# Kernel optimization log

Hardware: AMD Instinct MI355X
Metric: run time of the kernel (lower is better)

## Reference

```python
import jax, jax.numpy as jnp
import numpy as np

C = 128          # num_channels
HID = 256        # mlp hidden = 2*C
HEAD_DIM = 16    # C // num_heads (8)
SCALE = 1.0 / np.sqrt(HEAD_DIM)
EPS = 1e-5


def _linear_init(key, fan_in, fan_out):
    kw, kb = jax.random.split(key)
    s = 1.0 / np.sqrt(fan_in)
    w = jax.random.uniform(kw, (fan_in, fan_out), minval=-s, maxval=s, dtype=jnp.float32)
    b = jax.random.uniform(kb, (fan_out,), minval=-s, maxval=s, dtype=jnp.float32)
    return w, b


def setup_inputs() -> dict:
    key = jax.random.key(0)
    ks = jax.random.split(key, 8)
    x = jax.random.normal(ks[0], (4, C, 64, 64), dtype=jnp.float32)
    wq, bq = _linear_init(ks[1], C, C)
    wk, bk = _linear_init(ks[2], C, C)
    wv, bv = _linear_init(ks[3], C, C)
    wo, bo = _linear_init(ks[4], C, C)
    w1, b1 = _linear_init(ks[5], C, HID)
    w2, b2 = _linear_init(ks[6], HID, C)
    return {
        "x": x,
        "ln1_w": jnp.ones((C,), jnp.float32), "ln1_b": jnp.zeros((C,), jnp.float32),
        "wq": wq, "bq": bq, "wk": wk, "bk": bk, "wv": wv, "bv": bv,
        "wo": wo, "bo": bo,
        "ln2_w": jnp.ones((C,), jnp.float32), "ln2_b": jnp.zeros((C,), jnp.float32),
        "w1": w1, "b1": b1, "w2": w2, "b2": b2,
    }


def _layernorm(x, w, b):
    mu = jnp.mean(x, axis=-1, keepdims=True)
    var = jnp.mean(jnp.square(x - mu), axis=-1, keepdims=True)
    return (x - mu) * jax.lax.rsqrt(var + EPS) * w + b


def reference(x, ln1_w, ln1_b, wq, bq, wk, bk, wv, bv, wo, bo, ln2_w, ln2_b, w1, b1, w2, b2):
    B, Cc, H, W = x.shape
    t = x.reshape(B, Cc, H * W).transpose(0, 2, 1)  # [B, S, C]
    xl = _layernorm(t, ln1_w, ln1_b)
    q = xl @ wq + bq
    k = xl @ wk + bk
    v = xl @ wv + bv
    scores = jnp.einsum('bqc,bkc->bqk', q, k) * SCALE  # [B, S, S]
    # Faithful to source: softmax over dim=1 (the QUERY axis).
    attn = jax.nn.softmax(scores, axis=1)
    att_out = jnp.einsum('bqk,bkc->bqc', attn, v) @ wo + bo
    t = att_out + t
    m = _layernorm(t, ln2_w, ln2_b) @ w1 + b1
    m = jax.nn.gelu(m, approximate=False) @ w2 + b2
    t = jax.nn.gelu(m, approximate=False) + t  # second GELU per source
    return t.transpose(0, 2, 1).reshape(B, Cc, H, W)
```

## Files before the change

kernel.cpp:

```cpp
#include <hip/hip_runtime.h>
#include <math.h>

#define S 4096
#define CNUM 128
#define BATCH 4
#define MTOT (BATCH * S)
#define SCLOG2E 0.36067376022224085f
#define EPSLN 1e-5f
#define KSPLIT 8
#define QSPLIT 8

typedef __attribute__((ext_vector_type(8))) short bf16x8;
typedef __attribute__((ext_vector_type(4))) float f32x4;
typedef __attribute__((ext_vector_type(4))) unsigned int u32x4;

__device__ __forceinline__ float gelu_exact(float x) {
    return 0.5f * x * (1.0f + erff(x * 0.7071067811865476f));
}

__device__ __forceinline__ unsigned short f2b(float f) {
    union { float f; unsigned int u; } v; v.f = f;
    unsigned int r = (v.u + 0x7FFFu + ((v.u >> 16) & 1u)) >> 16;
    return (unsigned short)r;
}
__device__ __forceinline__ unsigned short f2b_ru(float f) {
    return (unsigned short)((__float_as_uint(f) + 0x8000u) >> 16);
}
__device__ __forceinline__ float b2f(unsigned short u) {
    return __uint_as_float((unsigned)u << 16);
}

__device__ __forceinline__ void gl_lds16(const void* g, void* l) {
    __builtin_amdgcn_global_load_lds(
        (__attribute__((address_space(1))) void*)g,
        (__attribute__((address_space(3))) void*)l, 16, 0, 0);
}

__global__ __launch_bounds__(256) void ln1_transpose(
    const float* __restrict__ x, const float* __restrict__ w, const float* __restrict__ bb,
    unsigned short* __restrict__ xlh, float* __restrict__ t)
{
    __shared__ float tile[128][65];
    __shared__ float mu[64], rs[64];
    const int b = blockIdx.y;
    const int s0 = blockIdx.x * 64;
    const float* xb = x + (size_t)b * CNUM * S;
    for (int i = threadIdx.x; i < 128 * 64; i += 256) {
        int c = i >> 6, sl = i & 63;
        tile[c][sl] = xb[(size_t)c * S + s0 + sl];
    }
    __syncthreads();
    if (threadIdx.x < 64) {
        float sum = 0.f, sq = 0.f;
        for (int c = 0; c < 128; ++c) {
            float v = tile[c][threadIdx.x];
            sum += v; sq += v * v;
        }
        float m = sum * (1.f / 128.f);
        float var = sq * (1.f / 128.f) - m * m;
        mu[threadIdx.x] = m;
        rs[threadIdx.x] = rsqrtf(var + EPSLN);
    }
    __syncthreads();
    for (int i = threadIdx.x; i < 128 * 64; i += 256) {
        int c = i & 127, sl = i >> 7;
        float v = tile[c][sl];
        size_t idx = ((size_t)b * S + s0 + sl) * CNUM + c;
        t[idx] = v;
        xlh[idx] = f2b((v - mu[sl]) * rs[sl] * w[c] + bb[c]);
    }
}

__global__ __launch_bounds__(256) void convw(
    const float* __restrict__ wq, const float* __restrict__ wk, const float* __restrict__ wv,
    const float* __restrict__ wo, const float* __restrict__ w1, const float* __restrict__ w2,
    const float* __restrict__ bq, const float* __restrict__ bk, const float* __restrict__ bv,
    unsigned short* __restrict__ wqkvh, unsigned short* __restrict__ woh,
    unsigned short* __restrict__ w1h, unsigned short* __restrict__ w2h,
    float* __restrict__ bqkv)
{
    int a = blockIdx.y;
    int idx = blockIdx.x * 256 + threadIdx.x;
    if (a == 6) {
        if (idx < 128) bqkv[idx] = bq[idx];
        else if (idx < 256) bqkv[idx] = bk[idx - 128];
        else if (idx < 384) bqkv[idx] = bv[idx - 256];
        return;
    }
    const float* src; unsigned short* dst; int Nsh, Ksz;
    switch (a) {
        case 0: src = wq; dst = wqkvh;          Nsh = 7; Ksz = 128; break;
        case 1: src = wk; dst = wqkvh + 16384;  Nsh = 7; Ksz = 128; break;
        case 2: src = wv; dst = wqkvh + 32768;  Nsh = 7; Ksz = 128; break;
        case 3: src = wo; dst = woh;            Nsh = 7; Ksz = 128; break;
        case 4: src = w1; dst = w1h;            Nsh = 8; Ksz = 128; break;
        default: src = w2; dst = w2h;           Nsh = 7; Ksz = 256; break;
    }
    int total = Ksz << Nsh;
    if (idx >= total) return;
    int k = idx >> Nsh, n = idx & ((1 << Nsh) - 1);
    dst[n * Ksz + k] = f2b(src[idx]);
}

template<int KT, int EPI>
__global__ __launch_bounds__(256) void gemm_mfma(
    const unsigned short* __restrict__ A, const unsigned short* __restrict__ Bt,
    const float* __restrict__ bias, const float* __restrict__ res,
    void* __restrict__ Cv, void* __restrict__ Cv2,
    const float* __restrict__ wln, const float* __restrict__ bln, int N)
{
    constexpr int CH = KT / 8;
    constexpr int CSH = (KT == 128) ? 4 : 5;
    __shared__ unsigned short As[64 * KT];
    __shared__ unsigned short Bs[128 * KT];
    __shared__ float2 lnred[2][64];
    const int bm = blockIdx.y * 64;
    const int bn = blockIdx.x * 128;
    const int z = blockIdx.z;
    const unsigned short* Btz = (EPI == 7) ? Bt + z * 16384 : Bt;
    const float* biasz = (EPI == 7) ? bias + z * 128 : bias;
    const int tid = threadIdx.x;
    const int w = tid >> 6, l = tid & 63;
    const int rw = (w & 1) * 32, cw = (w >> 1) * 64;
    const int lm = l & 15, lq = l >> 4;

    #pragma unroll
    for (int i = 0; i < (64 * CH) / 256; ++i) {
        int cid = i * 256 + tid;
        int r = cid >> CSH, c = cid & (CH - 1);
        int p = (c & ~15) | ((c ^ r) & 15);
        *(ulonglong2*)(As + r * KT + p * 8) =
            *(const ulonglong2*)(A + (size_t)(bm + r) * KT + c * 8);
    }
    #pragma unroll
    for (int i = 0; i < (128 * CH) / 256; ++i) {
        int cid = i * 256 + tid;
        int r = cid >> CSH, c = cid & (CH - 1);
        int p = (c & ~15) | ((c ^ r) & 15);
        *(ulonglong2*)(Bs + r * KT + p * 8) =
            *(const ulonglong2*)(Btz + (size_t)(bn + r) * KT + c * 8);
    }
    __syncthreads();

    f32x4 zero = {0.f, 0.f, 0.f, 0.f};
    f32x4 acc[2][4];
    #pragma unroll
    for (int i = 0; i < 2; ++i)
        #pragma unroll
        for (int j = 0; j < 4; ++j) acc[i][j] = zero;

    #pragma unroll
    for (int ks = 0; ks < KT / 32; ++ks) {
        int c_lin = ks * 4 + lq;
        bf16x8 a[2], bfr[4];
        #pragma unroll
        for (int i = 0; i < 2; ++i) {
            int m = rw + i * 16 + lm;
            int p = (c_lin & ~15) | ((c_lin ^ m) & 15);
            a[i] = *(const bf16x8*)(As + m * KT + p * 8);
        }
        #pragma unroll
        for (int j = 0; j < 4; ++j) {
            int n = cw + j * 16 + lm;
            int p = (c_lin & ~15) | ((c_lin ^ n) & 15);
            bfr[j] = *(const bf16x8*)(Bs + n * KT + p * 8);
        }
        #pragma unroll
        for (int i = 0; i < 2; ++i)
            #pragma unroll
            for (int j = 0; j < 4; ++j)
                acc[i][j] = __builtin_amdgcn_mfma_f32_16x16x32_bf16(a[i], bfr[j], acc[i][j], 0, 0, 0);
    }

    if (EPI == 3) {
        float vv[2][4][4];
        #pragma unroll
        for (int i = 0; i < 2; ++i) {
            int rowbase = bm + rw + i * 16 + lq * 4;
            #pragma unroll
            for (int j = 0; j < 4; ++j) {
                int col = bn + cw + j * 16 + lm;
                #pragma unroll
                for (int reg = 0; reg < 4; ++reg)
                    vv[i][j][reg] = acc[i][j][reg] + biasz[col] +
                                    res[(size_t)(rowbase + reg) * N + col];
            }
        }
        #pragma unroll
        for (int i = 0; i < 2; ++i)
            #pragma unroll
            for (int reg = 0; reg < 4; ++reg) {
                float s = 0.f, q = 0.f;
                #pragma unroll
                for (int j = 0; j < 4; ++j) {
                    float xv = vv[i][j][reg];
                    s += xv; q += xv * xv;
                }
                #pragma unroll
                for (int off = 1; off < 16; off <<= 1) {
                    s += __shfl_xor(s, off);
                    q += __shfl_xor(q, off);
                }
                if (lm == 0) {
                    float2 sq2; sq2.x = s; sq2.y = q;
                    lnred[cw >> 6][rw + i * 16 + lq * 4 + reg] = sq2;
                }
            }
        __syncthreads();
        #pragma unroll
        for (int i = 0; i < 2; ++i) {
            #pragma unroll
            for (int reg = 0; reg < 4; ++reg) {
                int lrow = rw + i * 16 + lq * 4 + reg;
                int row = bm + lrow;
                float2 h0 = lnred[0][lrow], h1 = lnred[1][lrow];
                float mean = (h0.x + h1.x) * (1.f / 128.f);
                float var  = (h0.y + h1.y) * (1.f / 128.f) - mean * mean;
                float rs = rsqrtf(var + EPSLN);
                #pragma unroll
                for (int j = 0; j < 4; ++j) {
                    int col = bn + cw + j * 16 + lm;
                    float xv = vv[i][j][reg];
                    ((float*)Cv)[(size_t)row * N + col] = xv;
                    ((unsigned short*)Cv2)[(size_t)row * N + col] =
                        f2b((xv - mean) * rs * wln[col] + bln[col]);
                }
            }
        }
        return;
    }

    #pragma unroll
    for (int i = 0; i < 2; ++i) {
        int rowbase = bm + rw + i * 16 + lq * 4;
        #pragma unroll
        for (int j = 0; j < 4; ++j) {
            int col = bn + cw + j * 16 + lm;
            float v[4];
            #pragma unroll
            for (int reg = 0; reg < 4; ++reg) v[reg] = acc[i][j][reg] + biasz[col];
            if (EPI == 6) {
                #pragma unroll
                for (int reg = 0; reg < 4; ++reg)
                    ((unsigned short*)Cv)[(size_t)(rowbase + reg) * N + col] = f2b(gelu_exact(v[reg]));
            } else if (EPI == 8) {
                int bb = rowbase >> 12, s = rowbase & 4095;
                float4 o;
                o.x = gelu_exact(v[0]) + res[(size_t)(rowbase + 0) * N + col];
                o.y = gelu_exact(v[1]) + res[(size_t)(rowbase + 1) * N + col];
                o.z = gelu_exact(v[2]) + res[(size_t)(rowbase + 2) * N + col];
                o.w = gelu_exact(v[3]) + res[(size_t)(rowbase + 3) * N + col];
                *(float4*)(((float*)Cv) + ((size_t)(bb * 128 + col)) * 4096 + s) = o;
            } else if (EPI == 7) {
                if (z < 2) {
                    unsigned short* dst = ((unsigned short*)Cv) + (size_t)z * MTOT * 128;
                    #pragma unroll
                    for (int reg = 0; reg < 4; ++reg)
                        dst[(size_t)(rowbase + reg) * 128 + col] = f2b(v[reg]);
                } else {
                    int bb = rowbase >> 12, s = rowbase & 4095;
                    int kc = s >> 6, g = (s >> 3) & 7;
                    ushort4 o;
                    o.x = f2b(v[0]); o.y = f2b(v[1]); o.z = f2b(v[2]); o.w = f2b(v[3]);
                    *(ushort4*)(((unsigned short*)Cv) + (size_t)2 * MTOT * 128 +
                                (((size_t)bb * 64 + kc) << 13) +
                                col * 64 + ((g ^ (col & 7)) << 3) + (s & 7)) = o;
                }
            }
        }
    }
}

__global__ __launch_bounds__(256) void colsum(
    const unsigned short* __restrict__ qh, const unsigned short* __restrict__ kh,
    float* __restrict__ psum_all)
{
    __shared__ unsigned short Qs[128 * 128];
    __shared__ unsigned short Ks[128 * 128];
    __shared__ float csum[2][128];
    const int b = blockIdx.z;
    const unsigned short* Q = qh + (size_t)b * S * 128;
    const unsigned short* Km = kh + (size_t)b * S * 128;
    const int bn = blockIdx.x * 128;
    const int q0 = blockIdx.y * (S / QSPLIT);
    const int tid = threadIdx.x;
    const int w = tid >> 6, l = tid & 63;
    const int wr = (w >> 1) * 64, wc = (w & 1) * 64;
    const int lm = l & 15, lq = l >> 4;

    #pragma unroll
    for (int i = 0; i < 8; ++i) {
        int cid = i * 256 + tid;
        int r = cid >> 4, c = cid & 15;
        int p = c ^ (r & 15);
        *(ulonglong2*)(Ks + r * 128 + p * 8) =
            *(const ulonglong2*)(Km + (size_t)(bn + r) * 128 + c * 8);
    }

    float jsum[4] = {0.f, 0.f, 0.f, 0.f};
    for (int qt = 0; qt < (S / QSPLIT) / 128; ++qt) {
        __syncthreads();
        #pragma unroll
        for (int i = 0; i < 8; ++i) {
            int cid = i * 256 + tid;
            int r = cid >> 4, c = cid & 15;
            int p = c ^ (r & 15);
            *(ulonglong2*)(Qs + r * 128 + p * 8) =
                *(const ulonglong2*)(Q + (size_t)(q0 + qt * 128 + r) * 128 + c * 8);
        }
        __syncthreads();

        f32x4 zero = {0.f, 0.f, 0.f, 0.f};
        f32x4 acc[4][4];
        #pragma unroll
        for (int i = 0; i < 4; ++i)
            #pragma unroll
            for (int j = 0; j < 4; ++j) acc[i][j] = zero;

        #pragma unroll
        for (int ks = 0; ks < 4; ++ks) {
            bf16x8 a[4], bfr[4];
            #pragma unroll
            for (int i = 0; i < 4; ++i) {
                int m = wr + i * 16 + lm;
                int p = (ks * 4 + lq) ^ (m & 15);
                a[i] = *(const bf16x8*)(Qs + m * 128 + p * 8);
            }
            #pragma unroll
            for (int j = 0; j < 4; ++j) {
                int n = wc + j * 16 + lm;
                int p = (ks * 4 + lq) ^ (n & 15);
                bfr[j] = *(const bf16x8*)(Ks + n * 128 + p * 8);
            }
            #pragma unroll
            for (int i = 0; i < 4; ++i)
                #pragma unroll
                for (int j = 0; j < 4; ++j)
                    acc[i][j] = __builtin_amdgcn_mfma_f32_16x16x32_bf16(a[i], bfr[j], acc[i][j], 0, 0, 0);
        }

        #pragma unroll
        for (int i = 0; i < 4; ++i)
            #pragma unroll
            for (int j = 0; j < 4; ++j)
                #pragma unroll
                for (int reg = 0; reg < 4; ++reg)
                    jsum[j] += b2f(f2b_ru(exp2f(acc[i][j][reg] * SCLOG2E)));
    }

    #pragma unroll
    for (int j = 0; j < 4; ++j) {
        jsum[j] += __shfl_xor(jsum[j], 16);
        jsum[j] += __shfl_xor(jsum[j], 32);
    }
    if (l < 16) {
        #pragma unroll
        for (int j = 0; j < 4; ++j)
            csum[w >> 1][wc + j * 16 + l] = jsum[j];
    }
    __syncthreads();
    if (tid < 128)
        psum_all[((size_t)(blockIdx.y * BATCH + b)) * S + bn + tid] = csum[0][tid] + csum[1][tid];
}

__global__ __launch_bounds__(256) void vscale(
    unsigned short* __restrict__ Vimg_all, const float* __restrict__ psum_all)
{
    const int b = blockIdx.z;
    unsigned short* Vimg = Vimg_all + (size_t)b * CNUM * S;
    int i = (blockIdx.x * 256 + threadIdx.x) * 4;
    int kc = i >> 13;
    int off = i & 8191;
    int c = off >> 6;
    int p = (off >> 3) & 7;
    int g = p ^ (c & 7);
    int k = kc * 64 + g * 8 + (off & 7);
    float4 L = *(const float4*)(psum_all + (size_t)b * S + k);
    #pragma unroll
    for (int t = 1; t < QSPLIT; ++t) {
        float4 Lt = *(const float4*)(psum_all + ((size_t)(t * BATCH + b)) * S + k);
        L.x += Lt.x; L.y += Lt.y; L.z += Lt.z; L.w += Lt.w;
    }
    ushort4 v = *(ushort4*)(Vimg + i);
    v.x = f2b(b2f(v.x) / L.x);
    v.y = f2b(b2f(v.y) / L.y);
    v.z = f2b(b2f(v.z) / L.z);
    v.w = f2b(b2f(v.w) / L.w);
    *(ushort4*)(Vimg + i) = v;
}

__global__ __launch_bounds__(256, 2) void fused_attnv(
    const unsigned short* __restrict__ qh, const unsigned short* __restrict__ kh,
    const unsigned short* __restrict__ Vimg_all, unsigned short* __restrict__ parts)
{
    __shared__ unsigned short Ks[32 * 128];
    __shared__ unsigned short Vls[128 * 64];
    __shared__ unsigned int   Ps[4][32 * 16];
    const int b = blockIdx.z;
    const unsigned short* Qm = qh + (size_t)b * S * 128;
    const unsigned short* Km = kh + (size_t)b * S * 128;
    const unsigned short* Vimg = Vimg_all + (((size_t)b * 64) << 13);
    unsigned short* Pout = parts + (size_t)blockIdx.x * ((size_t)MTOT * CNUM)
                                 + (size_t)b * S * CNUM;
    const int q0 = blockIdx.y * 128;
    const int kb0 = blockIdx.x * (S / KSPLIT);
    const int kc0 = blockIdx.x * (S / KSPLIT / 64);
    const int tid = threadIdx.x;
    const int w = tid >> 6, l = tid & 63;
    const int lm = l & 15, lq = l >> 4;
    const int row0 = q0 + w * 32;
    unsigned int* Pw = Ps[w];

    bf16x8 aq[2][4];
    #pragma unroll
    for (int i = 0; i < 2; ++i)
        #pragma unroll
        for (int ks = 0; ks < 4; ++ks)
            aq[i][ks] = *(const bf16x8*)(Qm + (size_t)(row0 + i * 16 + lm) * 128 + (ks * 4 + lq) * 8);

    f32x4 zero = {0.f, 0.f, 0.f, 0.f};
    f32x4 acco[2][8];
    #pragma unroll
    for (int i = 0; i < 2; ++i)
        #pragma unroll
        for (int j = 0; j < 8; ++j) acco[i][j] = zero;

    for (int kt = 0; kt < S / KSPLIT / 32; ++kt) {
        const int kb = kb0 + kt * 32;
        __syncthreads();
        #pragma unroll
        for (int i2 = 0; i2 < 2; ++i2) {
            int cid = i2 * 256 + tid;
            int r = cid >> 4, c = cid & 15;
            int p = c ^ (r & 15);
            *(ulonglong2*)(Ks + r * 128 + p * 8) =
                *(const ulonglong2*)(Km + (size_t)(kb + r) * 128 + c * 8);
        }
        if ((kt & 1) == 0) {
            const unsigned short* src = Vimg + ((size_t)(kc0 + (kt >> 1)) << 13) + tid * 8;
            #pragma unroll
            for (int i2 = 0; i2 < 4; ++i2)
                gl_lds16(src + i2 * 2048, &Vls[(i2 * 256 + tid) * 8]);
        }
        __syncthreads();

        f32x4 accT[2][2];
        #pragma unroll
        for (int ki = 0; ki < 2; ++ki)
            #pragma unroll
            for (int qj = 0; qj < 2; ++qj) accT[ki][qj] = zero;
        #pragma unroll
        for (int ks = 0; ks < 4; ++ks) {
            bf16x8 kfr[2];
            #pragma unroll
            for (int ki = 0; ki < 2; ++ki) {
                int n = ki * 16 + lm;
                int p = (ks * 4 + lq) ^ (n & 15);
                kfr[ki] = *(const bf16x8*)(Ks + n * 128 + p * 8);
            }
            #pragma unroll
            for (int ki = 0; ki < 2; ++ki)
                #pragma unroll
                for (int qj = 0; qj < 2; ++qj)
                    accT[ki][qj] = __builtin_amdgcn_mfma_f32_16x16x32_bf16(kfr[ki], aq[qj][ks], accT[ki][qj], 0, 0, 0);
        }

        #pragma unroll
        for (int qj = 0; qj < 2; ++qj) {
            unsigned int* pw = Pw + (qj * 16 + lm) * 16;
            #pragma unroll
            for (int ki = 0; ki < 2; ++ki)
                #pragma unroll
                for (int r2 = 0; r2 < 2; ++r2) {
                    float e0 = exp2f(accT[ki][qj][2 * r2]     * SCLOG2E);
                    float e1 = exp2f(accT[ki][qj][2 * r2 + 1] * SCLOG2E);
                    unsigned int pk;
                    asm("v_cvt_pk_bf16_f32 %0, %1, %2" : "=v"(pk) : "v"(e0), "v"(e1));
                    pw[(ki * 8 + lq * 2 + r2) ^ lm] = pk;
                }
        }

        bf16x8 ap[2];
        #pragma unroll
        for (int i = 0; i < 2; ++i) {
            const unsigned int* pr = Pw + (i * 16 + lm) * 16;
            u32x4 uu = { pr[(lq * 4 + 0) ^ lm], pr[(lq * 4 + 1) ^ lm],
                         pr[(lq * 4 + 2) ^ lm], pr[(lq * 4 + 3) ^ lm] };
            ap[i] = __builtin_bit_cast(bf16x8, uu);
        }
        const int vh = (kt & 1) * 4;
        #pragma unroll
        for (int j = 0; j < 8; ++j) {
            int n = j * 16 + lm;
            bf16x8 bv = *(const bf16x8*)(Vls + n * 64 + (((vh + lq) ^ (n & 7)) << 3));
            acco[0][j] = __builtin_amdgcn_mfma_f32_16x16x32_bf16(ap[0], bv, acco[0][j], 0, 0, 0);
            acco[1][j] = __builtin_amdgcn_mfma_f32_16x16x32_bf16(ap[1], bv, acco[1][j], 0, 0, 0);
        }
    }

    #pragma unroll
    for (int i = 0; i < 2; ++i) {
        int rowb = row0 + i * 16 + lq * 4;
        #pragma unroll
        for (int j = 0; j < 8; ++j) {
            int col = j * 16 + lm;
            #pragma unroll
            for (int reg = 0; reg < 4; ++reg)
                Pout[(size_t)(rowb + reg) * CNUM + col] = f2b(acco[i][j][reg]);
        }
    }
}

__global__ __launch_bounds__(256) void reduce8b(
    const ushort4* __restrict__ parts, ushort4* __restrict__ dst)
{
    size_t i = (size_t)blockIdx.x * 256 + threadIdx.x;
    const size_t stride = (size_t)MTOT * CNUM / 4;
    float sx = 0.f, sy = 0.f, sz = 0.f, sw = 0.f;
    #pragma unroll
    for (int p = 0; p < KSPLIT; ++p) {
        ushort4 v = parts[i + p * stride];
        sx += b2f(v.x); sy += b2f(v.y); sz += b2f(v.z); sw += b2f(v.w);
    }
    ushort4 o;
    o.x = f2b(sx); o.y = f2b(sy); o.z = f2b(sz); o.w = f2b(sw);
    dst[i] = o;
}

extern "C" void kernel_launch(void* const* d_in, const int* in_sizes, int n_in,
                              void* d_out, int out_size, void* d_ws, size_t ws_size,
                              hipStream_t stream)
{
    (void)in_sizes; (void)n_in; (void)out_size; (void)ws_size;
    const float* x    = (const float*)d_in[0];
    const float* ln1w = (const float*)d_in[1];
    const float* ln1b = (const float*)d_in[2];
    const float* wq   = (const float*)d_in[3];
    const float* bq   = (const float*)d_in[4];
    const float* wk   = (const float*)d_in[5];
    const float* bk   = (const float*)d_in[6];
    const float* wv   = (const float*)d_in[7];
    const float* bv   = (const float*)d_in[8];
    const float* wo   = (const float*)d_in[9];
    const float* bo   = (const float*)d_in[10];
    const float* ln2w = (const float*)d_in[11];
    const float* ln2b = (const float*)d_in[12];
    const float* w1   = (const float*)d_in[13];
    const float* b1   = (const float*)d_in[14];
    const float* w2   = (const float*)d_in[15];
    const float* b2   = (const float*)d_in[16];
    float* out = (float*)d_out;

    float* ws = (float*)d_ws;
    const size_t NSC = (size_t)MTOT * CNUM;
    float* t      = ws;
    float* y      = t + NSC;
    float* psum   = y + NSC;
    unsigned short* parts = (unsigned short*)(psum + (size_t)QSPLIT * BATCH * S);
    unsigned short* xlh = parts + (size_t)KSPLIT * NSC;
    unsigned short* qh  = xlh + NSC;
    unsigned short* kh  = qh + NSC;
    unsigned short* Vt  = kh + NSC;
    unsigned short* attouth = Vt + NSC;
    unsigned short* zh  = attouth + NSC;
    unsigned short* hh  = zh + NSC;
    unsigned short* wqkvh = hh + (size_t)MTOT * 256;
    unsigned short* woh = wqkvh + 3 * 16384;
    unsigned short* w1h = woh + 16384;
    unsigned short* w2h = w1h + 32768;
    float* bqkv = (float*)(w2h + 32768);

    ln1_transpose<<<dim3(S / 64, BATCH), 256, 0, stream>>>(x, ln1w, ln1b, xlh, t);
    convw<<<dim3(128, 7), 256, 0, stream>>>(wq, wk, wv, wo, w1, w2, bq, bk, bv,
                                            wqkvh, woh, w1h, w2h, bqkv);

    gemm_mfma<128, 7><<<dim3(1, MTOT / 64, 3), 256, 0, stream>>>(
        xlh, wqkvh, bqkv, nullptr, qh, nullptr, nullptr, nullptr, 128);

    colsum<<<dim3(S / 128, QSPLIT, BATCH), 256, 0, stream>>>(qh, kh, psum);
    vscale<<<dim3(CNUM * S / 4 / 256, 1, BATCH), 256, 0, stream>>>(Vt, psum);
    fused_attnv<<<dim3(KSPLIT, S / 128, BATCH), 256, 0, stream>>>(qh, kh, Vt, parts);
    reduce8b<<<NSC / 4 / 256, 256, 0, stream>>>((const ushort4*)parts, (ushort4*)attouth);

    gemm_mfma<128, 3><<<dim3(1, MTOT / 64), 256, 0, stream>>>(
        attouth, woh, bo, t, y, zh, ln2w, ln2b, 128);
    gemm_mfma<128, 6><<<dim3(2, MTOT / 64), 256, 0, stream>>>(
        zh, w1h, b1, nullptr, hh, nullptr, nullptr, nullptr, 256);
    gemm_mfma<256, 8><<<dim3(1, MTOT / 64), 256, 0, stream>>>(
        hh, w2h, b2, y, out, nullptr, nullptr, nullptr, 128);
}
```

Baseline: 246.8 us.

## Switch attention-V kernel to 32x32 MFMA with register P and direct V loads

```diff
diff --git a/kernel.cpp b/kernel.cpp
--- a/kernel.cpp
+++ b/kernel.cpp
@@ -12,6 +12,7 @@
 
 typedef __attribute__((ext_vector_type(8))) short bf16x8;
 typedef __attribute__((ext_vector_type(4))) float f32x4;
+typedef __attribute__((ext_vector_type(16))) float f32x16;
 typedef __attribute__((ext_vector_type(4))) unsigned int u32x4;
 
 __device__ __forceinline__ float gelu_exact(float x) {
@@ -28,12 +29,6 @@
 }
 __device__ __forceinline__ float b2f(unsigned short u) {
     return __uint_as_float((unsigned)u << 16);
-}
-
-__device__ __forceinline__ void gl_lds16(const void* g, void* l) {
-    __builtin_amdgcn_global_load_lds(
-        (__attribute__((address_space(1))) void*)g,
-        (__attribute__((address_space(3))) void*)l, 16, 0, 0);
 }
 
 __global__ __launch_bounds__(256) void ln1_transpose(
@@ -259,12 +254,10 @@
                         dst[(size_t)(rowbase + reg) * 128 + col] = f2b(v[reg]);
                 } else {
                     int bb = rowbase >> 12, s = rowbase & 4095;
-                    int kc = s >> 6, g = (s >> 3) & 7;
                     ushort4 o;
                     o.x = f2b(v[0]); o.y = f2b(v[1]); o.z = f2b(v[2]); o.w = f2b(v[3]);
                     *(ushort4*)(((unsigned short*)Cv) + (size_t)2 * MTOT * 128 +
-                                (((size_t)bb * 64 + kc) << 13) +
-                                col * 64 + ((g ^ (col & 7)) << 3) + (s & 7)) = o;
+                                ((size_t)(bb * 128 + col)) * 4096 + s) = o;
                 }
             }
         }
@@ -364,151 +357,125 @@
 }
 
 __global__ __launch_bounds__(256) void vscale(
-    unsigned short* __restrict__ Vimg_all, const float* __restrict__ psum_all)
+    unsigned short* __restrict__ Vt_all, const float* __restrict__ psum_all)
 {
     const int b = blockIdx.z;
-    unsigned short* Vimg = Vimg_all + (size_t)b * CNUM * S;
+    unsigned short* Vt = Vt_all + (size_t)b * CNUM * S;
     int i = (blockIdx.x * 256 + threadIdx.x) * 4;
-    int kc = i >> 13;
-    int off = i & 8191;
-    int c = off >> 6;
-    int p = (off >> 3) & 7;
-    int g = p ^ (c & 7);
-    int k = kc * 64 + g * 8 + (off & 7);
+    int k = i & (S - 1);
     float4 L = *(const float4*)(psum_all + (size_t)b * S + k);
     #pragma unroll
     for (int t = 1; t < QSPLIT; ++t) {
         float4 Lt = *(const float4*)(psum_all + ((size_t)(t * BATCH + b)) * S + k);
         L.x += Lt.x; L.y += Lt.y; L.z += Lt.z; L.w += Lt.w;
     }
-    ushort4 v = *(ushort4*)(Vimg + i);
+    ushort4 v = *(ushort4*)(Vt + i);
     v.x = f2b(b2f(v.x) / L.x);
     v.y = f2b(b2f(v.y) / L.y);
     v.z = f2b(b2f(v.z) / L.z);
     v.w = f2b(b2f(v.w) / L.w);
-    *(ushort4*)(Vimg + i) = v;
-}
-
-__global__ __launch_bounds__(256, 2) void fused_attnv(
+    *(ushort4*)(Vt + i) = v;
+}
+
+__global__ __launch_bounds__(256, 3) void fused_attnv(
     const unsigned short* __restrict__ qh, const unsigned short* __restrict__ kh,
-    const unsigned short* __restrict__ Vimg_all, unsigned short* __restrict__ parts)
+    const unsigned short* __restrict__ Vt_all, unsigned short* __restrict__ parts)
 {
     __shared__ unsigned short Ks[32 * 128];
-    __shared__ unsigned short Vls[128 * 64];
-    __shared__ unsigned int   Ps[4][32 * 16];
     const int b = blockIdx.z;
     const unsigned short* Qm = qh + (size_t)b * S * 128;
     const unsigned short* Km = kh + (size_t)b * S * 128;
-    const unsigned short* Vimg = Vimg_all + (((size_t)b * 64) << 13);
+    const unsigned short* Vb = Vt_all + (size_t)b * CNUM * S;
     unsigned short* Pout = parts + (size_t)blockIdx.x * ((size_t)MTOT * CNUM)
                                  + (size_t)b * S * CNUM;
     const int q0 = blockIdx.y * 128;
     const int kb0 = blockIdx.x * (S / KSPLIT);
-    const int kc0 = blockIdx.x * (S / KSPLIT / 64);
     const int tid = threadIdx.x;
     const int w = tid >> 6, l = tid & 63;
-    const int lm = l & 15, lq = l >> 4;
+    const int lc = l & 31, lh = l >> 5;
     const int row0 = q0 + w * 32;
-    unsigned int* Pw = Ps[w];
-
-    bf16x8 aq[2][4];
-    #pragma unroll
-    for (int i = 0; i < 2; ++i)
-        #pragma unroll
-        for (int ks = 0; ks < 4; ++ks)
-            aq[i][ks] = *(const bf16x8*)(Qm + (size_t)(row0 + i * 16 + lm) * 128 + (ks * 4 + lq) * 8);
-
-    f32x4 zero = {0.f, 0.f, 0.f, 0.f};
-    f32x4 acco[2][8];
-    #pragma unroll
-    for (int i = 0; i < 2; ++i)
-        #pragma unroll
-        for (int j = 0; j < 8; ++j) acco[i][j] = zero;
+
+    bf16x8 aq[8];
+    #pragma unroll
+    for (int d = 0; d < 8; ++d)
+        aq[d] = *(const bf16x8*)(Qm + (size_t)(row0 + lc) * 128 + d * 16 + lh * 8);
+
+    f32x16 acco[4];
+    #pragma unroll
+    for (int cb = 0; cb < 4; ++cb)
+        #pragma unroll
+        for (int r = 0; r < 16; ++r) acco[cb][r] = 0.f;
+
+    const unsigned short* vrow = Vb + (size_t)lc * S + lh * 8;
 
     for (int kt = 0; kt < S / KSPLIT / 32; ++kt) {
         const int kb = kb0 + kt * 32;
-        __syncthreads();
+
+        bf16x8 v0[4];
+        #pragma unroll
+        for (int cb = 0; cb < 4; ++cb)
+            v0[cb] = *(const bf16x8*)(vrow + (size_t)cb * 32 * S + kb);
+
+        if (kt) __syncthreads();
         #pragma unroll
         for (int i2 = 0; i2 < 2; ++i2) {
             int cid = i2 * 256 + tid;
             int r = cid >> 4, c = cid & 15;
-            int p = c ^ (r & 15);
-            *(ulonglong2*)(Ks + r * 128 + p * 8) =
+            *(ulonglong2*)(Ks + r * 128 + ((c ^ (r & 15)) * 8)) =
                 *(const ulonglong2*)(Km + (size_t)(kb + r) * 128 + c * 8);
         }
-        if ((kt & 1) == 0) {
-            const unsigned short* src = Vimg + ((size_t)(kc0 + (kt >> 1)) << 13) + tid * 8;
-            #pragma unroll
-            for (int i2 = 0; i2 < 4; ++i2)
-                gl_lds16(src + i2 * 2048, &Vls[(i2 * 256 + tid) * 8]);
-        }
         __syncthreads();
 
-        f32x4 accT[2][2];
-        #pragma unroll
-        for (int ki = 0; ki < 2; ++ki)
-            #pragma unroll
-            for (int qj = 0; qj < 2; ++qj) accT[ki][qj] = zero;
-        #pragma unroll
-        for (int ks = 0; ks < 4; ++ks) {
-            bf16x8 kfr[2];
-            #pragma unroll
-            for (int ki = 0; ki < 2; ++ki) {
-                int n = ki * 16 + lm;
-                int p = (ks * 4 + lq) ^ (n & 15);
-                kfr[ki] = *(const bf16x8*)(Ks + n * 128 + p * 8);
-            }
-            #pragma unroll
-            for (int ki = 0; ki < 2; ++ki)
-                #pragma unroll
-                for (int qj = 0; qj < 2; ++qj)
-                    accT[ki][qj] = __builtin_amdgcn_mfma_f32_16x16x32_bf16(kfr[ki], aq[qj][ks], accT[ki][qj], 0, 0, 0);
-        }
-
-        #pragma unroll
-        for (int qj = 0; qj < 2; ++qj) {
-            unsigned int* pw = Pw + (qj * 16 + lm) * 16;
-            #pragma unroll
-            for (int ki = 0; ki < 2; ++ki)
-                #pragma unroll
-                for (int r2 = 0; r2 < 2; ++r2) {
-                    float e0 = exp2f(accT[ki][qj][2 * r2]     * SCLOG2E);
-                    float e1 = exp2f(accT[ki][qj][2 * r2 + 1] * SCLOG2E);
-                    unsigned int pk;
-                    asm("v_cvt_pk_bf16_f32 %0, %1, %2" : "=v"(pk) : "v"(e0), "v"(e1));
-                    pw[(ki * 8 + lq * 2 + r2) ^ lm] = pk;
-                }
-        }
-
-        bf16x8 ap[2];
-        #pragma unroll
-        for (int i = 0; i < 2; ++i) {
-            const unsigned int* pr = Pw + (i * 16 + lm) * 16;
-            u32x4 uu = { pr[(lq * 4 + 0) ^ lm], pr[(lq * 4 + 1) ^ lm],
-                         pr[(lq * 4 + 2) ^ lm], pr[(lq * 4 + 3) ^ lm] };
-            ap[i] = __builtin_bit_cast(bf16x8, uu);
-        }
-        const int vh = (kt & 1) * 4;
-        #pragma unroll
-        for (int j = 0; j < 8; ++j) {
-            int n = j * 16 + lm;
-            bf16x8 bv = *(const bf16x8*)(Vls + n * 64 + (((vh + lq) ^ (n & 7)) << 3));
-            acco[0][j] = __builtin_amdgcn_mfma_f32_16x16x32_bf16(ap[0], bv, acco[0][j], 0, 0, 0);
-            acco[1][j] = __builtin_amdgcn_mfma_f32_16x16x32_bf16(ap[1], bv, acco[1][j], 0, 0, 0);
-        }
-    }
-
-    #pragma unroll
-    for (int i = 0; i < 2; ++i) {
-        int rowb = row0 + i * 16 + lq * 4;
-        #pragma unroll
-        for (int j = 0; j < 8; ++j) {
-            int col = j * 16 + lm;
-            #pragma unroll
-            for (int reg = 0; reg < 4; ++reg)
-                Pout[(size_t)(rowb + reg) * CNUM + col] = f2b(acco[i][j][reg]);
-        }
-    }
+        f32x16 accT;
+        #pragma unroll
+        for (int r = 0; r < 16; ++r) accT[r] = 0.f;
+        #pragma unroll
+        for (int d = 0; d < 8; ++d) {
+            int slot = d * 2 + lh;
+            bf16x8 kf = *(const bf16x8*)(Ks + lc * 128 + ((slot ^ (lc & 15)) * 8));
+            accT = __builtin_amdgcn_mfma_f32_32x32x16_bf16(kf, aq[d], accT, 0, 0, 0);
+        }
+
+        bf16x8 v1[4];
+        #pragma unroll
+        for (int cb = 0; cb < 4; ++cb)
+            v1[cb] = *(const bf16x8*)(vrow + (size_t)cb * 32 * S + kb + 16);
+
+        unsigned int pk[4][2];
+        #pragma unroll
+        for (int t = 0; t < 4; ++t)
+            #pragma unroll
+            for (int p = 0; p < 2; ++p) {
+                float e0 = exp2f(accT[t * 4 + 2 * p]     * SCLOG2E);
+                float e1 = exp2f(accT[t * 4 + 2 * p + 1] * SCLOG2E);
+                asm("v_cvt_pk_bf16_f32 %0, %1, %2" : "=v"(pk[t][p]) : "v"(e0), "v"(e1));
+            }
+        #pragma unroll
+        for (int p = 0; p < 2; ++p) {
+            asm volatile("v_permlane32_swap_b32 %0, %1" : "+v"(pk[0][p]), "+v"(pk[1][p]));
+            asm volatile("v_permlane32_swap_b32 %0, %1" : "+v"(pk[2][p]), "+v"(pk[3][p]));
+        }
+        u32x4 u0 = {pk[0][0], pk[0][1], pk[1][0], pk[1][1]};
+        u32x4 u1 = {pk[2][0], pk[2][1], pk[3][0], pk[3][1]};
+        bf16x8 ap0 = __builtin_bit_cast(bf16x8, u0);
+        bf16x8 ap1 = __builtin_bit_cast(bf16x8, u1);
+
+        __builtin_amdgcn_s_setprio(1);
+        #pragma unroll
+        for (int cb = 0; cb < 4; ++cb) {
+            acco[cb] = __builtin_amdgcn_mfma_f32_32x32x16_bf16(ap0, v0[cb], acco[cb], 0, 0, 0);
+            acco[cb] = __builtin_amdgcn_mfma_f32_32x32x16_bf16(ap1, v1[cb], acco[cb], 0, 0, 0);
+        }
+        __builtin_amdgcn_s_setprio(0);
+    }
+
+    #pragma unroll
+    for (int cb = 0; cb < 4; ++cb)
+        #pragma unroll
+        for (int r = 0; r < 16; ++r) {
+            int q = (r & 3) + 8 * (r >> 2) + 4 * lh;
+            Pout[(size_t)(row0 + q) * CNUM + cb * 32 + lc] = f2b(acco[cb][r]);
+        }
 }
 
 __global__ __launch_bounds__(256) void reduce8b(
```

Result: slower. 286.8 us (+16.2%).
